# Performance work log

Hardware: AMD Instinct MI355X
Metric: run time of the kernel (lower is better)

The kernel has to match this reference:

```python
import jax, jax.numpy as jnp
import numpy as np
from jax import lax

SAMPLING_RATE = 44100.0


def setup_inputs() -> dict:
    key = jax.random.key(0)
    k_x, k_w1, k_w2 = jax.random.split(key, 3)
    T, B, F = 44100, 32, 1
    S, H = 16, 64
    x = jax.random.normal(k_x, (T, B, F), dtype=jnp.float32)
    # small init so the Euler integration stays numerically tame over 44k steps
    W1 = jax.random.normal(k_w1, (F + S, H), dtype=jnp.float32) * 0.1
    b1 = jnp.zeros((H,), dtype=jnp.float32)
    W2 = jax.random.normal(k_w2, (H, S), dtype=jnp.float32) * 0.1
    b2 = jnp.zeros((S,), dtype=jnp.float32)
    return {"x": x, "W1": W1, "b1": b1, "W2": W2, "b2": b2}


def reference(x, W1, b1, W2, b2):
    # ScaledODENetFE forward Euler: y0 = sr * state (state starts at zeros),
    # y1 = y0 + f(t0, y0/sr), stored trajectory is y1/sr, output is feature 0.
    sr = jnp.asarray(SAMPLING_RATE, dtype=x.dtype)
    T, B, F = x.shape
    S = W2.shape[1]
    y0 = jnp.zeros((B, S), dtype=x.dtype)  # sr * zeros initial state

    def step(y_carry, x_t):  # x_t: (B, F)
        inp = jnp.concatenate([x_t, y_carry / sr], axis=-1)  # (B, F+S)
        d = jnp.tanh(inp @ W1 + b1) @ W2 + b2                # (B, S)
        y1 = y_carry + d
        return y1, y1 / sr

    _, ys = lax.scan(step, y0, x[:-1])                        # (T-1, B, S)
    y_full = jnp.concatenate([jnp.zeros((1, B, S), dtype=x.dtype), ys], axis=0)
    return y_full[:, :, 0:1]                                  # (T, B, 1)
```

## Files before the change

### kernel.cpp

```cpp
#include <hip/hip_runtime.h>


#define SRATE 44100.0f
#define T_TOTAL 44100
#define BATCH 32
#define HID 64
#define ST 16
#define KSCALE 2.8853900817779268f

typedef float v2f __attribute__((ext_vector_type(2)));

template <int CTRL>
__device__ __forceinline__ float dppmov(float x) {
    return __builtin_bit_cast(float,
        __builtin_amdgcn_update_dpp(0, __builtin_bit_cast(int, x),
                                    CTRL, 0xF, 0xF, false));
}

__device__ __forceinline__ float bcast(float v, int lane) {
    return __builtin_bit_cast(float,
        __builtin_amdgcn_readlane(__builtin_bit_cast(int, v), lane));
}

__device__ __forceinline__ int parity(int v) { return __builtin_popcount(v) & 1; }

__global__ __launch_bounds__(64, 1)
void ScaledODENetFE_kernel(const float* __restrict__ x,
                           const float* __restrict__ W1,
                           const float* __restrict__ b1,
                           const float* __restrict__ W2,
                           const float* __restrict__ b2v,
                           float* __restrict__ out) {
    const int b = blockIdx.x;
    const int lane = threadIdx.x;
    const int TM1 = T_TOTAL - 1;
    const int NFULL = 689;

    const float w1xK = W1[lane] * KSCALE;
    float w1yd[ST];
    #pragma unroll
    for (int s = 0; s < ST; ++s)
        w1yd[s] = (W1[(1 + s) * HID + lane] / SRATE) * KSCALE;

    float C2 = 0.f;
    #pragma unroll
    for (int s = 0; s < ST; ++s) C2 = fmaf(b2v[s], w1yd[s], C2);
    float pconst0 = 0.f;
    for (int s = 0; s < ST; ++s) {
        float pc = 0.f;
        for (int k = 0; k < HID; ++k) pc += W2[k * ST + s];
        C2 = fmaf(pc, w1yd[s], C2);
        if (s == 0) pconst0 = pc;
    }
    v2f wy2[8];
    #pragma unroll
    for (int m = 0; m < 8; ++m) wy2[m] = (v2f){w1yd[2 * m], w1yd[2 * m + 1]};
    const v2f C2v = (v2f){C2, 0.f};

    const int p1 = parity(lane & 5), p2 = parity(lane & 6);
    const int p3 = (lane >> 2) & 1, p4 = (lane >> 3) & 1;
    float wA[8], wB[8];
    #pragma unroll
    for (int j = 0; j < 8; ++j) {
        const int i = 2 * j;
        const int c1 = (i & 1) ^ p1;
        const int c2 = ((i >> 1) & 1) ^ p2;
        const int c3 = ((i >> 2) & 1) ^ p3;
        const int c4 = ((i >> 3) & 1) ^ p4;
        const int s = (c1 ? 1 : 0) ^ (c2 ? 2 : 0) ^ (c3 ? 7 : 0) ^ (c4 ? 8 : 0);
        wA[j] = -2.f * W2[lane * ST + s];
        wB[j] = -2.f * W2[(lane ^ 1) * ST + s];
    }
    v2f wA2[4], wB2[4];
    #pragma unroll
    for (int m = 0; m < 4; ++m) {
        wA2[m] = (v2f){wA[2 * m], wA[2 * m + 1]};
        wB2[m] = (v2f){wB[2 * m], wB[2 * m + 1]};
    }

    const int bp32 = ((lane ^ 32) & 63) << 2;
    const int bp48 = ((lane ^ 48) & 63) << 2;
    const float b20 = b2v[0];

    float V  = b1[lane] * KSCALE;
    float y0 = 0.f;

    if (lane == 0) out[b] = 0.f;

    float xv = x[lane * BATCH + b];
    float z = fmaf(bcast(xv, 0), w1xK, V);

    auto STEP = [&](float xtn, float& pb0) {
        float t = __builtin_amdgcn_exp2f(z);
        float r = __builtin_amdgcn_rcpf(t + 1.f);

        float zbase = fmaf(xtn, w1xK, V);

        float rx = dppmov<0xB1>(r);
        v2f r2v = (v2f){r, r};
        v2f rx2 = (v2f){rx, rx};
        v2f u1p[4];
        #pragma unroll
        for (int m = 0; m < 4; ++m)
            u1p[m] = __builtin_elementwise_fma(rx2, wB2[m], r2v * wA2[m]);

        float u2[4];
        #pragma unroll
        for (int m = 0; m < 4; ++m)
            u2[m] = u1p[m].x + dppmov<0x4E>(u1p[m].y);

        float u3a = u2[0] + dppmov<0x141>(u2[1]);
        float u3b = u2[2] + dppmov<0x141>(u2[3]);

        float Pb = u3a + dppmov<0x128>(u3b);

        int   Pi  = __builtin_bit_cast(int, Pb);
        float a16 = __builtin_bit_cast(float,
                    __builtin_amdgcn_ds_swizzle(Pi, 0x401F));
        float a32 = __builtin_bit_cast(float,
                    __builtin_amdgcn_ds_bpermute(bp32, Pi));
        float a48 = __builtin_bit_cast(float,
                    __builtin_amdgcn_ds_bpermute(bp48, Pi));
        float Pc = (Pb + a16) + (a32 + a48);

        v2f p01 = (v2f){bcast(Pc, 0),  bcast(Pc, 1)};
        v2f p23 = (v2f){bcast(Pc, 2),  bcast(Pc, 3)};
        v2f p45 = (v2f){bcast(Pc, 4),  bcast(Pc, 5)};
        v2f p67 = (v2f){bcast(Pc, 6),  bcast(Pc, 7)};
        v2f p89 = (v2f){bcast(Pc, 8),  bcast(Pc, 9)};
        v2f pAB = (v2f){bcast(Pc, 10), bcast(Pc, 11)};
        v2f pCD = (v2f){bcast(Pc, 12), bcast(Pc, 13)};
        v2f pEF = (v2f){bcast(Pc, 14), bcast(Pc, 15)};
        v2f acc_a = __builtin_elementwise_fma(p01, wy2[0], C2v);
        acc_a = __builtin_elementwise_fma(p23, wy2[1], acc_a);
        acc_a = __builtin_elementwise_fma(p45, wy2[2], acc_a);
        acc_a = __builtin_elementwise_fma(p67, wy2[3], acc_a);
        v2f acc_b = p89 * wy2[4];
        acc_b = __builtin_elementwise_fma(pAB, wy2[5], acc_b);
        acc_b = __builtin_elementwise_fma(pCD, wy2[6], acc_b);
        acc_b = __builtin_elementwise_fma(pEF, wy2[7], acc_b);
        v2f accs = acc_a + acc_b;
        float R = accs.x + accs.y;

        pb0 = p01.x;
        z = zbase + R;
        V = V + R;
    };

    for (int blk = 0; blk < NFULL; ++blk) {
        const int t0 = blk * 64;
        float xvn = x[min(t0 + 64 + lane, TM1 - 1) * BATCH + b];
        float outy = 0.f;
        float pb0;

        #pragma unroll 9
        for (int kk = 0; kk < 63; ++kk) {
            STEP(bcast(xv, kk + 1), pb0);
            y0 += pconst0 + pb0;
            outy = (kk == lane) ? y0 : outy;
        }
        STEP(bcast(xvn, 0), pb0);
        y0 += pconst0 + pb0;
        outy = (63 == lane) ? y0 : outy;

        const int n = t0 + 1 + lane;
        out[n * BATCH + b] = fmaf((float)n, b20, outy) / SRATE;
        xv = xvn;
    }

    {
        const int t0 = NFULL * 64;
        float outy = 0.f;
        float pb0;
        #pragma unroll
        for (int kk = 0; kk < 3; ++kk) {
            STEP(bcast(xv, kk + 1), pb0);
            y0 += pconst0 + pb0;
            outy = (kk == lane) ? y0 : outy;
        }
        if (lane < 3) {
            const int n = t0 + 1 + lane;
            out[n * BATCH + b] = fmaf((float)n, b20, outy) / SRATE;
        }
    }
}

extern "C" void kernel_launch(void* const* d_in, const int* in_sizes, int n_in,
                              void* d_out, int out_size, void* d_ws, size_t ws_size,
                              hipStream_t stream) {
    const float* x  = (const float*)d_in[0];
    const float* W1 = (const float*)d_in[1];
    const float* b1 = (const float*)d_in[2];
    const float* W2 = (const float*)d_in[3];
    const float* b2 = (const float*)d_in[4];
    float* out = (float*)d_out;

    ScaledODENetFE_kernel<<<BATCH, 64, 0, stream>>>(x, W1, b1, W2, b2, out);
}
```

Before: 6.625 ms.

## Interleave two independent batch recurrences per wavefront to hide latency

Each block now runs two batch elements, interleaving their serial Euler-step chains so that the latency of one chain's transcendental, DPP, swizzle and readlane operations can be overlapped with the other's. The grid shrinks from 32 to 16 single-wave blocks. This trades parallelism across CUs (unused anyway) for instruction-level parallelism within a wave, at the cost of more registers and twice the instructions per wave.

```diff
diff --git a/kernel.cpp b/kernel.cpp
--- a/kernel.cpp
+++ b/kernel.cpp
@@ -31,7 +31,8 @@
                            const float* __restrict__ W2,
                            const float* __restrict__ b2v,
                            float* __restrict__ out) {
-    const int b = blockIdx.x;
+    const int b0 = 2 * blockIdx.x;
+    const int b1i = b0 + 1;
     const int lane = threadIdx.x;
     const int TM1 = T_TOTAL - 1;
     const int NFULL = 689;
@@ -82,15 +83,17 @@
     const int bp48 = ((lane ^ 48) & 63) << 2;
     const float b20 = b2v[0];
 
-    float V  = b1[lane] * KSCALE;
-    float y0 = 0.f;
-
-    if (lane == 0) out[b] = 0.f;
-
-    float xv = x[lane * BATCH + b];
-    float z = fmaf(bcast(xv, 0), w1xK, V);
-
-    auto STEP = [&](float xtn, float& pb0) {
+    float VA = b1[lane] * KSCALE, VB = VA;
+    float y0A = 0.f, y0B = 0.f;
+
+    if (lane == 0) { out[b0] = 0.f; out[b1i] = 0.f; }
+
+    float xvA = x[lane * BATCH + b0];
+    float xvB = x[lane * BATCH + b1i];
+    float zA = fmaf(bcast(xvA, 0), w1xK, VA);
+    float zB = fmaf(bcast(xvB, 0), w1xK, VB);
+
+    auto STEP = [&](float& z, float& V, float xtn, float& pb0) {
         float t = __builtin_amdgcn_exp2f(z);
         float r = __builtin_amdgcn_rcpf(t + 1.f);
 
@@ -149,38 +152,52 @@
 
     for (int blk = 0; blk < NFULL; ++blk) {
         const int t0 = blk * 64;
-        float xvn = x[min(t0 + 64 + lane, TM1 - 1) * BATCH + b];
-        float outy = 0.f;
-        float pb0;
+        const int nidx = min(t0 + 64 + lane, TM1 - 1) * BATCH;
+        float xvnA = x[nidx + b0];
+        float xvnB = x[nidx + b1i];
+        float outyA = 0.f, outyB = 0.f;
+        float pb0A, pb0B;
 
         #pragma unroll 9
         for (int kk = 0; kk < 63; ++kk) {
-            STEP(bcast(xv, kk + 1), pb0);
-            y0 += pconst0 + pb0;
-            outy = (kk == lane) ? y0 : outy;
+            STEP(zA, VA, bcast(xvA, kk + 1), pb0A);
+            STEP(zB, VB, bcast(xvB, kk + 1), pb0B);
+            y0A += pconst0 + pb0A;
+            outyA = (kk == lane) ? y0A : outyA;
+            y0B += pconst0 + pb0B;
+            outyB = (kk == lane) ? y0B : outyB;
         }
-        STEP(bcast(xvn, 0), pb0);
-        y0 += pconst0 + pb0;
-        outy = (63 == lane) ? y0 : outy;
+        STEP(zA, VA, bcast(xvnA, 0), pb0A);
+        y0A += pconst0 + pb0A;
+        outyA = (63 == lane) ? y0A : outyA;
+        STEP(zB, VB, bcast(xvnB, 0), pb0B);
+        y0B += pconst0 + pb0B;
+        outyB = (63 == lane) ? y0B : outyB;
 
         const int n = t0 + 1 + lane;
-        out[n * BATCH + b] = fmaf((float)n, b20, outy) / SRATE;
-        xv = xvn;
+        out[n * BATCH + b0]  = fmaf((float)n, b20, outyA) / SRATE;
+        out[n * BATCH + b1i] = fmaf((float)n, b20, outyB) / SRATE;
+        xvA = xvnA;
+        xvB = xvnB;
     }
 
     {
         const int t0 = NFULL * 64;
-        float outy = 0.f;
-        float pb0;
+        float outyA = 0.f, outyB = 0.f;
+        float pb0A, pb0B;
         #pragma unroll
         for (int kk = 0; kk < 3; ++kk) {
-            STEP(bcast(xv, kk + 1), pb0);
-            y0 += pconst0 + pb0;
-            outy = (kk == lane) ? y0 : outy;
+            STEP(zA, VA, bcast(xvA, kk + 1), pb0A);
+            STEP(zB, VB, bcast(xvB, kk + 1), pb0B);
+            y0A += pconst0 + pb0A;
+            outyA = (kk == lane) ? y0A : outyA;
+            y0B += pconst0 + pb0B;
+            outyB = (kk == lane) ? y0B : outyB;
         }
         if (lane < 3) {
             const int n = t0 + 1 + lane;
-            out[n * BATCH + b] = fmaf((float)n, b20, outy) / SRATE;
+            out[n * BATCH + b0]  = fmaf((float)n, b20, outyA) / SRATE;
+            out[n * BATCH + b1i] = fmaf((float)n, b20, outyB) / SRATE;
         }
     }
 }
@@ -195,5 +212,5 @@
     const float* b2 = (const float*)d_in[4];
     float* out = (float*)d_out;
 
-    ScaledODENetFE_kernel<<<BATCH, 64, 0, stream>>>(x, W1, b1, W2, b2, out);
-}
+    ScaledODENetFE_kernel<<<BATCH / 2, 64, 0, stream>>>(x, W1, b1, W2, b2, out);
+}
```

After: 11.96 ms. 1.81x slower.
